# Kernel tuning notes

Hardware: AMD Instinct MI355X
Metric: run time of the kernel (lower is better)

The kernel has to match this reference:

```python
import jax, jax.numpy as jnp
import numpy as np

B, D_IN, D_OUT, DICT = 2048, 768, 768, 24576
TOP_K, TOP_K_AUX = 32, 512
L1_COEFF, AUX_PENALTY, N_DEAD = 0.001, 0.03125, 100.0


def setup_inputs() -> dict:
    key = jax.random.key(0)
    k1, k2, k3, k4, k5, k6 = jax.random.split(key, 6)
    x_in = jax.random.normal(k1, (B, D_IN), dtype=jnp.float32)
    y_target = jax.random.normal(k2, (B, D_OUT), dtype=jnp.float32)
    nb = jax.random.randint(k3, (DICT,), 0, 200).astype(jnp.float32)
    # kaiming-uniform-ish init
    bound_e = float(np.sqrt(6.0 / D_IN))
    W_enc = jax.random.uniform(k4, (D_IN, DICT), minval=-bound_e, maxval=bound_e, dtype=jnp.float32)
    bound_d = float(np.sqrt(6.0 / DICT))
    W_dec = jax.random.uniform(k5, (DICT, D_OUT), minval=-bound_d, maxval=bound_d, dtype=jnp.float32)
    W_dec = W_dec / jnp.linalg.norm(W_dec, axis=-1, keepdims=True)  # unit-norm rows
    b_dec = jnp.zeros((D_OUT,), dtype=jnp.float32)
    return {"x_in": x_in, "y_target": y_target, "num_batches_not_active": nb,
            "W_enc": W_enc, "W_dec": W_dec, "b_dec": b_dec}


def _unit_norm(x):
    m = x.mean(axis=-1, keepdims=True)
    x = x - m
    s = jnp.std(x, axis=-1, keepdims=True, ddof=1)  # torch .std is unbiased
    return x / (s + 1e-5), m, s


def reference(x_in, y_target, num_batches_not_active, W_enc, W_dec, b_dec):
    xn, _, _ = _unit_norm(x_in)
    yn, y_mean, y_std = _unit_norm(y_target)
    x_enc = xn - b_dec  # pre_enc_bias (input_size == output_size)
    acts = jax.nn.relu(x_enc @ W_enc)                      # [B, DICT]
    vals, idx = jax.lax.top_k(acts, TOP_K)                 # [B, TOP_K]
    rows = jnp.arange(B)[:, None]
    acts_sparse = jnp.zeros_like(acts).at[rows, idx].set(vals)
    y_pred = acts_sparse @ W_dec + b_dec                   # [B, D_OUT]
    y_pred_out = y_pred * y_std + y_mean

    # stateful dead-feature bookkeeping (update_inactive_features)
    col_active = acts_sparse.sum(axis=0) > 0
    nb = jnp.where(col_active, 0.0, num_batches_not_active + 1.0)

    l2_loss = jnp.mean((y_pred - yn) ** 2)
    l1_norm = jnp.mean(jnp.abs(acts_sparse).sum(axis=-1))
    l1_loss = L1_COEFF * l1_norm
    l0_norm = jnp.mean((acts_sparse > 0).astype(jnp.float32).sum(axis=-1))

    # auxiliary loss on dead features (static-shape masked top-k; masked cols
    # get -1 < relu acts so extras relu-clip to 0 -> same math as torch gather)
    dead = nb >= N_DEAD
    masked = jnp.where(dead[None, :], acts, -1.0)
    av, ai = jax.lax.top_k(masked, TOP_K_AUX)
    av = jax.nn.relu(av)
    acts_aux = jnp.zeros_like(acts).at[rows, ai].set(av)
    y_pred_aux = acts_aux @ W_dec
    residual = yn - y_pred
    l2_aux = AUX_PENALTY * jnp.mean((y_pred_aux - residual) ** 2)
    aux_loss = jnp.where(dead.any(), l2_aux, 0.0)

    loss = l2_loss + l1_loss + aux_loss
    num_dead_features = (nb > N_DEAD).sum()
    return (y_pred_out, acts_sparse, loss, l2_loss, l1_loss, l0_norm, l1_norm,
            aux_loss, num_dead_features)
```

## Files before the change

### kernel.cpp

```cpp
#include <hip/hip_runtime.h>
#include <math.h>

#define BATCH 2048
#define DIN 768
#define DICT 24576
#define KM 32
#define KA 512
#define NPT 48
#define L1_COEFF 0.001f
#define AUX_PENALTY 0.03125f
#define CAND_MAX 768
#define CAND_DELTA 0.08f
#define AUX_SPLIT 8
#define SAUX 18432
#define AGB ((DIN/128)*(BATCH/128)*AUX_SPLIT)

typedef __attribute__((ext_vector_type(8))) short bf16x8;
typedef __attribute__((ext_vector_type(8))) unsigned short u16x8;
typedef __attribute__((ext_vector_type(4))) float f32x4;

constexpr size_t WS_XENC   = 0;
constexpr size_t WS_YN     = WS_XENC + (size_t)BATCH*DIN;
constexpr size_t WS_YMEAN  = WS_YN + (size_t)BATCH*DIN;
constexpr size_t WS_YSTD   = WS_YMEAN + BATCH;
constexpr size_t WS_RES    = WS_YSTD + BATCH;
constexpr size_t WS_NSEL   = WS_RES + (size_t)BATCH*DIN;
constexpr size_t WS_SEL    = WS_NSEL + BATCH;
constexpr size_t WS_SELV   = WS_SEL + (size_t)BATCH*KM;
constexpr size_t WS_COLACT = WS_SELV + (size_t)BATCH*KM;
constexpr size_t WS_ACC    = WS_COLACT + DICT;
constexpr size_t WS_DB     = WS_ACC + 8;
constexpr size_t WS_XEB    = WS_DB + DICT/32;
constexpr size_t WS_WETF   = WS_XEB + (size_t)BATCH*DIN/2;
constexpr size_t WS_WETB   = WS_WETF + (size_t)DICT*DIN;
constexpr size_t WS_WDB    = WS_WETB + (size_t)DICT*DIN/2;
constexpr size_t WS_DPREF  = WS_XEB + DICT/32;
constexpr size_t WS_META   = WS_XEB + 2*(DICT/32);

__device__ __forceinline__ unsigned short f2b(float f){
    unsigned u = __float_as_uint(f);
    return (unsigned short)((u + 0x7fffu + ((u >> 16) & 1u)) >> 16);
}
__device__ __forceinline__ float b2f(unsigned short h){ return __uint_as_float(((unsigned)h) << 16); }

__device__ __forceinline__ void gld_lds16(const void* g, void* l){
    __builtin_amdgcn_global_load_lds(
        (const __attribute__((address_space(1))) unsigned int*)g,
        (__attribute__((address_space(3))) unsigned int*)l, 16, 0, 0);
}

__device__ __forceinline__ int blk_count512_w(int cw, int* s16, int par){
    if ((threadIdx.x & 63) == 0) s16[par*8 + (threadIdx.x >> 6)] = cw;
    __syncthreads();
    int tot = 0;
    #pragma unroll
    for (int w=0; w<8; w++) tot += s16[par*8+w];
    return tot;
}
__device__ __forceinline__ float blk_sum512(float v, float* s16, int par){
    #pragma unroll
    for (int off=32; off; off>>=1) v += __shfl_down(v, off);
    if ((threadIdx.x & 63) == 0) s16[par*8 + (threadIdx.x >> 6)] = v;
    __syncthreads();
    float t = 0.f;
    #pragma unroll
    for (int w=0; w<8; w++) t += s16[par*8+w];
    return t;
}
__device__ __forceinline__ float blk_sum256(float v, float* s8, int par){
    #pragma unroll
    for (int off=32; off; off>>=1) v += __shfl_down(v, off);
    if ((threadIdx.x & 63) == 0) s8[par*4 + (threadIdx.x >> 6)] = v;
    __syncthreads();
    float t = 0.f;
    #pragma unroll
    for (int w=0; w<4; w++) t += s8[par*4+w];
    return t;
}

__global__ __launch_bounds__(256) void prep_k(const float* __restrict__ x,
        const float* __restrict__ y, const float* __restrict__ bdec,
        const float* __restrict__ We, const float* __restrict__ Wd,
        float* __restrict__ Tf, unsigned short* __restrict__ Tb,
        unsigned short* __restrict__ Td, float* __restrict__ ws){
    __shared__ float s8[8];
    __shared__ float t1[32][33];
    __shared__ float t2[32][33];
    const int tid = threadIdx.x;
    if (blockIdx.x < 2*BATCH){
        int b = blockIdx.x; bool isy = b >= BATCH; int row = isy ? b - BATCH : b;
        if (b < 8){
            float* dst = ws + WS_COLACT;
            for (int i = b*256 + tid; i < DICT + 8; i += 2048) dst[i] = 0.f;
        }
        const float* src = (isy ? y : x) + (size_t)row*DIN;
        float v0 = src[tid], v1 = src[tid+256], v2 = src[tid+512];
        float s = blk_sum256(v0+v1+v2, s8, 0);
        float mean = s * (1.f/(float)DIN);
        float d0 = v0-mean, d1 = v1-mean, d2 = v2-mean;
        float vs = blk_sum256(d0*d0+d1*d1+d2*d2, s8, 1);
        float sd = sqrtf(vs / (float)(DIN-1));
        float inv = 1.f / (sd + 1e-5f);
        if (isy){
            float* yn = ws + WS_YN + (size_t)row*DIN;
            yn[tid] = d0*inv; yn[tid+256] = d1*inv; yn[tid+512] = d2*inv;
            if (tid==0){ ws[WS_YMEAN+row] = mean; ws[WS_YSTD+row] = sd; }
        } else {
            float* xe = ws + WS_XENC + (size_t)row*DIN;
            unsigned short* xeb = (unsigned short*)(ws + WS_XEB) + (size_t)row*DIN;
            float e0 = d0*inv - bdec[tid];
            float e1 = d1*inv - bdec[tid+256];
            float e2 = d2*inv - bdec[tid+512];
            xe[tid] = e0; xe[tid+256] = e1; xe[tid+512] = e2;
            xeb[tid] = f2b(e0); xeb[tid+256] = f2b(e1); xeb[tid+512] = f2b(e2);
        }
    } else {
        int t = blockIdx.x - 2*BATCH;
        int bx = t % (DICT/32), by = t / (DICT/32);
        int a0 = bx*32, k0 = by*32;
        int r = tid >> 5, c = tid & 31;
        #pragma unroll
        for (int rr=r; rr<32; rr+=8){
            t1[rr][c] = We[(size_t)(k0+rr)*DICT + a0 + c];
            t2[rr][c] = Wd[(size_t)(a0+rr)*DIN + k0 + c];
        }
        __syncthreads();
        #pragma unroll
        for (int rr=r; rr<32; rr+=8){
            float v = t1[c][rr];
            Tf[(size_t)(a0+rr)*DIN + k0 + c] = v;
            Tb[(size_t)(a0+rr)*DIN + k0 + c] = f2b(v);
            Td[(size_t)(k0+rr)*DICT + a0 + c] = f2b(t2[c][rr]);
        }
    }
}

__global__ __launch_bounds__(256) void gemm_mfma(const unsigned short* __restrict__ Abf,
        const unsigned short* __restrict__ Bbf, unsigned short* __restrict__ C){
    __shared__ __align__(16) unsigned short As[128*64];
    __shared__ __align__(16) unsigned short Bs[128*64];
    const int tid = threadIdx.x;
    const int w = tid >> 6, lane = tid & 63;
    const int g = blockIdx.x;
    const int xcd = g & 7;
    const int s_ = g >> 3;
    const int m_t = s_ & 15;
    const int n_t = xcd + 8*(s_ >> 4);
    const int m0 = m_t*128, n0 = n_t*128;
    const int srow = lane >> 3;
    const int schunk = (lane & 7) ^ srow;
    const int wm = (w >> 1)*64, wn = (w & 1)*64;
    f32x4 acc[16];
    #pragma unroll
    for (int i=0;i<16;i++) acc[i] = (f32x4){0.f,0.f,0.f,0.f};
    for (int kt = 0; kt < DIN; kt += 64){
        #pragma unroll
        for (int q=0;q<4;q++){
            int s = w*4 + q;
            int row = 8*s + srow;
            gld_lds16(Abf + (size_t)(m0+row)*DIN + kt + schunk*8, &As[8*s*64]);
            gld_lds16(Bbf + (size_t)(n0+row)*DIN + kt + schunk*8, &Bs[8*s*64]);
        }
        __syncthreads();
        #pragma unroll
        for (int kk=0; kk<64; kk+=32){
            bf16x8 af[4], bfr[4];
            int ch = (kk>>3) + (lane>>4);
            #pragma unroll
            for (int i=0;i<4;i++){
                int row = wm + i*16 + (lane&15);
                af[i] = *(const bf16x8*)&As[row*64 + ((ch ^ (row&7))<<3)];
            }
            #pragma unroll
            for (int j=0;j<4;j++){
                int row = wn + j*16 + (lane&15);
                bfr[j] = *(const bf16x8*)&Bs[row*64 + ((ch ^ (row&7))<<3)];
            }
            #pragma unroll
            for (int i=0;i<4;i++)
                #pragma unroll
                for (int j=0;j<4;j++)
                    acc[i*4+j] = __builtin_amdgcn_mfma_f32_16x16x32_bf16(af[i], bfr[j], acc[i*4+j], 0,0,0);
        }
        __syncthreads();
    }
    #pragma unroll
    for (int i=0;i<4;i++){
        #pragma unroll
        for (int r=0;r<4;r++){
            int m = m0 + wm + i*16 + (lane>>4)*4 + r;
            unsigned short* crow = C + (size_t)m*DICT + n0 + wn + (lane&15);
            #pragma unroll
            for (int j=0;j<4;j++)
                crow[j*16] = f2b(fmaxf(acc[i*4+j][r], 0.f) + 0.0f);
        }
    }
}

__global__ __launch_bounds__(512) void topk_main(const unsigned short* __restrict__ actsb,
        const float* __restrict__ WeTf, const float* __restrict__ Wdec,
        const float* __restrict__ bdec, float* __restrict__ ws,
        float* __restrict__ ypred_out){
    const int row = blockIdx.x, tid = threadIdx.x;
    const int lane = tid & 63, wid = tid >> 6;
    __shared__ float s_f16[16];
    __shared__ float s_x[DIN];
    __shared__ int   s_ci[CAND_MAX];
    __shared__ float s_cv[CAND_MAX];
    __shared__ int   s_li[KM];
    __shared__ float s_lv[KM];
    __shared__ int   s_n, s_m;
    const unsigned short* arow = actsb + (size_t)row * DICT;
    const float* xrow = ws + WS_XENC + (size_t)row * DIN;
    unsigned short h[NPT];
    #pragma unroll
    for (int i=0;i<6;i++){
        u16x8 v = *(const u16x8*)&arow[i*4096 + tid*8];
        #pragma unroll
        for (int e=0;e<8;e++) h[i*8+e] = v[e];
    }
    s_x[tid] = xrow[tid];
    if (tid < DIN-512) s_x[tid+512] = xrow[tid+512];
    if (tid == 0){ s_n = 0; s_m = 0; }

    unsigned prefix = 0;
    for (int bit=14; bit>=0; bit--){
        unsigned cand = prefix | (1u<<bit);
        int c = 0;
        #pragma unroll
        for (int q=0;q<NPT;q++) c += (int)__popcll(__ballot((unsigned)h[q] >= cand));
        if (c >= KM) prefix = cand;
    }
    float tc = b2f((unsigned short)prefix) - CAND_DELTA;
    __syncthreads();
    #pragma unroll
    for (int q=0;q<NPT;q++){
        if (b2f(h[q]) > tc){
            int p = atomicAdd(&s_n, 1);
            if (p < CAND_MAX) s_ci[p] = (q>>3)*4096 + tid*8 + (q&7);
        }
    }
    __syncthreads();
    int nc = s_n; if (nc > CAND_MAX) nc = CAND_MAX;
    for (int c = wid; c < nc; c += 8){
        const float* wr = WeTf + (size_t)s_ci[c]*DIN;
        float p = 0.f;
        #pragma unroll
        for (int t=0; t<12; t++) p = fmaf(s_x[lane + 64*t], wr[lane + 64*t], p);
        #pragma unroll
        for (int off=32; off; off>>=1) p += __shfl_down(p, off);
        if (lane == 0) s_cv[c] = fmaxf(p, 0.f);
    }
    __syncthreads();
    if (tid < nc){
        float vi = s_cv[tid]; int ii = s_ci[tid];
        int rank = 0;
        for (int j=0; j<nc; j++){
            float vj = s_cv[j];
            rank += (vj > vi) || (vj == vi && s_ci[j] < ii);
        }
        if (rank < KM){
            int p = atomicAdd(&s_m, 1);
            s_li[p] = ii; s_lv[p] = vi;
        }
    }
    __syncthreads();
    if (tid < KM){
        ((int*)ws)[WS_COLACT + s_li[tid]] = 1;
        ((int*)ws)[WS_SEL  + (size_t)row*KM + tid] = s_li[tid];
        ws[WS_SELV + (size_t)row*KM + tid] = s_lv[tid];
    }
    if (tid == 0){
        float l1 = 0.f; int l0 = 0;
        for (int l=0;l<KM;l++){ l1 += s_lv[l]; l0 += (s_lv[l] > 0.f); }
        atomicAdd(&ws[WS_ACC+1], l1);
        atomicAdd(&ws[WS_ACC+2], (float)l0);
    }
    __syncthreads();
    float ym = ws[WS_YMEAN+row], ys = ws[WS_YSTD+row];
    float l2loc = 0.f;
    for (int c = tid; c < DIN; c += 512){
        float acc = bdec[c];
        #pragma unroll 4
        for (int l=0;l<KM;l++) acc = fmaf(s_lv[l], Wdec[(size_t)s_li[l]*DIN + c], acc);
        float ynv = ws[WS_YN + (size_t)row*DIN + c];
        float d = acc - ynv;
        l2loc += d*d;
        ws[WS_RES + (size_t)row*DIN + c] = ynv - acc;
        ypred_out[(size_t)row*DIN + c] = fmaf(acc, ys, ym);
    }
    float l2t = blk_sum512(l2loc, s_f16, 0);
    if (tid==0) atomicAdd(&ws[WS_ACC+0], l2t);
}

__global__ __launch_bounds__(768) void deadscan_k(const float* __restrict__ nb,
        float* __restrict__ ws){
    __shared__ int s[DICT/32];
    __shared__ int c12[12];
    const int t = threadIdx.x;
    const int* colact = (const int*)ws + WS_COLACT;
    unsigned bits = 0; int cgt = 0;
    const int base = t*32;
    #pragma unroll 8
    for (int b=0;b<32;b++){
        int j = base + b;
        float nbn = colact[j] ? 0.f : nb[j] + 1.f;
        bits |= (nbn >= 100.f ? 1u : 0u) << b;
        cgt  += (nbn > 100.f) ? 1 : 0;
    }
    ((unsigned*)(ws + WS_DB))[t] = bits;
    int pc = __popc(bits);
    s[t] = pc;
    #pragma unroll
    for (int off=32; off; off>>=1) cgt += __shfl_down(cgt, off);
    if ((t & 63) == 0) c12[t >> 6] = cgt;
    __syncthreads();
    for (int off=1; off<DICT/32; off<<=1){
        int v = (t >= off) ? s[t-off] : 0;
        __syncthreads();
        s[t] += v;
        __syncthreads();
    }
    ((int*)(ws + WS_DPREF))[t] = s[t] - pc;
    if (t == DICT/32 - 1){
        int nd = s[t];
        int ndpad = (nd + 63) & ~63;
        if (ndpad > SAUX) ndpad = SAUX;
        int* meta = (int*)(ws + WS_META);
        meta[0] = nd; meta[1] = ndpad; meta[2] = ndpad >> 6;
        meta[3] = ((ndpad >> 6) + AUX_SPLIT - 1) / AUX_SPLIT;
        int tot = 0;
        #pragma unroll
        for (int wv=0; wv<12; wv++) tot += c12[wv];
        ws[WS_ACC+4] = (float)tot;
        ((int*)ws)[WS_ACC+5] = (nd > 0) ? 1 : 0;
    }
}

__global__ __launch_bounds__(512) void auxprep_k(const unsigned short* __restrict__ actsb,
        unsigned short* __restrict__ wdt, unsigned short* __restrict__ auxc,
        float* __restrict__ ws){
    __shared__ unsigned s_db[DICT/32];
    __shared__ int      s_dp[DICT/32];
    __shared__ int      s_i16[16];
    __shared__ unsigned short s_out[SAUX];
    const int tid = threadIdx.x;
    for (int i=tid; i<DICT/32; i+=512){
        s_db[i] = ((const unsigned*)(ws + WS_DB))[i];
        s_dp[i] = ((const int*)(ws + WS_DPREF))[i];
    }
    const int nd    = ((const int*)(ws + WS_META))[0];
    const int ndpad = ((const int*)(ws + WS_META))[1];
    __syncthreads();
    if (blockIdx.x < DIN){
        const int n = blockIdx.x;
        unsigned short* row = wdt + (size_t)n*DICT;
        #pragma unroll
        for (int i=0;i<6;i++){
            u16x8 a = *(const u16x8*)&row[i*4096 + tid*8];
            int w = i*128 + (tid>>2);
            unsigned dbw = s_db[w]; int dpw = s_dp[w];
            #pragma unroll
            for (int e=0;e<8;e++){
                int bit = (tid&3)*8 + e;
                if ((dbw >> bit) & 1u){
                    int p = dpw + __popc(dbw & ((1u<<bit)-1u));
                    if (p < SAUX) s_out[p] = a[e];
                }
            }
        }
        for (int t2 = nd + tid; t2 < ndpad; t2 += 512) s_out[t2] = 0;
        __syncthreads();
        for (int i = tid*8; i < ndpad; i += 4096)
            *(u16x8*)&row[i] = *(const u16x8*)&s_out[i];
    } else {
        const int row = blockIdx.x - DIN;
        const unsigned short* arow = actsb + (size_t)row * DICT;
        unsigned short key[NPT];
        #pragma unroll
        for (int i=0;i<6;i++){
            u16x8 v = *(const u16x8*)&arow[i*4096 + tid*8];
            unsigned dbw = s_db[i*128 + (tid>>2)];
            #pragma unroll
            for (int e=0;e<8;e++){
                unsigned short hv = v[e];
                key[i*8+e] = (((dbw >> ((tid&3)*8 + e)) & 1u) && hv) ? hv : 0;
            }
        }
        int par = 0;
        unsigned prefix = 0;
        for (int bit=14; bit>=0; bit--){
            unsigned cand = prefix | (1u<<bit);
            int c = 0;
            #pragma unroll
            for (int q=0;q<NPT;q++) c += (int)__popcll(__ballot((unsigned)key[q] >= cand));
            int tot = blk_count512_w(c, s_i16, par); par ^= 1;
            if (tot >= KA) prefix = cand;
        }
        unsigned thr = prefix ? prefix : 1u;
        #pragma unroll
        for (int i=0;i<6;i++){
            int w = i*128 + (tid>>2);
            unsigned dbw = s_db[w];
            int dpw = s_dp[w];
            #pragma unroll
            for (int e=0;e<8;e++){
                int bit = (tid&3)*8 + e;
                if ((dbw >> bit) & 1u){
                    int p = dpw + __popc(dbw & ((1u<<bit)-1u));
                    unsigned short kv = key[i*8+e];
                    if (p < SAUX) s_out[p] = ((unsigned)kv >= thr) ? kv : (unsigned short)0;
                }
            }
        }
        for (int t2 = nd + tid; t2 < ndpad; t2 += 512) s_out[t2] = 0;
        __syncthreads();
        unsigned short* crow = auxc + (size_t)row * SAUX;
        for (int i = tid*8; i < ndpad; i += 4096)
            *(u16x8*)&crow[i] = *(const u16x8*)&s_out[i];
    }
}

__global__ __launch_bounds__(256) void auxgz_k(const unsigned short* __restrict__ Abf,
        const unsigned short* __restrict__ Bbf, float* __restrict__ ws,
        float* __restrict__ acts){
    __shared__ __align__(16) unsigned short As[128*64];
    __shared__ __align__(16) unsigned short Bs[128*64];
    const int tid = threadIdx.x;
    if (blockIdx.x >= AGB){
        const int row = blockIdx.x - AGB;
        float4 z = make_float4(0.f,0.f,0.f,0.f);
        float4* arow4 = (float4*)(acts + (size_t)row*DICT);
        #pragma unroll
        for (int i=0;i<24;i++) arow4[tid + 256*i] = z;
        __syncthreads();
        if (tid < KM){
            int j   = ((const int*)ws)[WS_SEL + (size_t)row*KM + tid];
            float v = ws[WS_SELV + (size_t)row*KM + tid];
            (acts + (size_t)row*DICT)[j] = v;
        }
        return;
    }
    const int nkt   = ((const int*)(ws + WS_META))[2];
    const int chunk = ((const int*)(ws + WS_META))[3];
    const int g = blockIdx.x;
    const int z = g & 7;
    const int s_ = g >> 3;
    const int m_t = s_ & 15;
    const int n_t = s_ >> 4;
    int t0 = z * chunk;
    int t1 = t0 + chunk; if (t1 > nkt) t1 = nkt;
    const int w = tid >> 6, lane = tid & 63;
    const int m0 = m_t*128, n0 = n_t*128;
    const int srow = lane >> 3;
    const int schunk = (lane & 7) ^ srow;
    const int wm = (w >> 1)*64, wn = (w & 1)*64;
    f32x4 acc[16];
    #pragma unroll
    for (int i=0;i<16;i++) acc[i] = (f32x4){0.f,0.f,0.f,0.f};
    for (int t = t0; t < t1; ++t){
        int kt = t*64;
        #pragma unroll
        for (int q=0;q<4;q++){
            int s = w*4 + q;
            int row = 8*s + srow;
            gld_lds16(Abf + (size_t)(m0+row)*SAUX + kt + schunk*8, &As[8*s*64]);
            gld_lds16(Bbf + (size_t)(n0+row)*DICT + kt + schunk*8, &Bs[8*s*64]);
        }
        __syncthreads();
        #pragma unroll
        for (int kk=0; kk<64; kk+=32){
            bf16x8 af[4], bfr[4];
            int ch = (kk>>3) + (lane>>4);
            #pragma unroll
            for (int i=0;i<4;i++){
                int row = wm + i*16 + (lane&15);
                af[i] = *(const bf16x8*)&As[row*64 + ((ch ^ (row&7))<<3)];
            }
            #pragma unroll
            for (int j=0;j<4;j++){
                int row = wn + j*16 + (lane&15);
                bfr[j] = *(const bf16x8*)&Bs[row*64 + ((ch ^ (row&7))<<3)];
            }
            #pragma unroll
            for (int i=0;i<4;i++)
                #pragma unroll
                for (int j=0;j<4;j++)
                    acc[i*4+j] = __builtin_amdgcn_mfma_f32_16x16x32_bf16(af[i], bfr[j], acc[i*4+j], 0,0,0);
        }
        __syncthreads();
    }
    float* buf = ws + ((z < 6) ? (WS_WETB + (size_t)z*BATCH*DIN)
                               : (z == 6 ? WS_YN : WS_XENC));
    #pragma unroll
    for (int i=0;i<4;i++){
        #pragma unroll
        for (int r=0;r<4;r++){
            int m = m0 + wm + i*16 + (lane>>4)*4 + r;
            float* crow = buf + (size_t)m*DIN + n0 + wn + (lane&15);
            #pragma unroll
            for (int j=0;j<4;j++) crow[j*16] = acc[i*4+j][r];
        }
    }
}

__global__ __launch_bounds__(256) void auxloss_k(float* __restrict__ ws){
    __shared__ float s8[8];
    const float4* b0 = (const float4*)(ws + WS_WETB);
    const float4* b1 = (const float4*)(ws + WS_WETB + 1*(size_t)BATCH*DIN);
    const float4* b2 = (const float4*)(ws + WS_WETB + 2*(size_t)BATCH*DIN);
    const float4* b3 = (const float4*)(ws + WS_WETB + 3*(size_t)BATCH*DIN);
    const float4* b4 = (const float4*)(ws + WS_WETB + 4*(size_t)BATCH*DIN);
    const float4* b5 = (const float4*)(ws + WS_WETB + 5*(size_t)BATCH*DIN);
    const float4* b6 = (const float4*)(ws + WS_YN);
    const float4* b7 = (const float4*)(ws + WS_XENC);
    const float4* r4 = (const float4*)(ws + WS_RES);
    float s = 0.f;
    const size_t n4 = (size_t)BATCH*DIN/4;
    for (size_t i = (size_t)blockIdx.x*256 + threadIdx.x; i < n4; i += (size_t)gridDim.x*256){
        float4 a0 = b0[i], a1 = b1[i], a2 = b2[i], a3 = b3[i];
        float4 a4 = b4[i], a5 = b5[i], a6 = b6[i], a7 = b7[i];
        float4 rr = r4[i];
        float x0 = ((a0.x+a1.x)+(a2.x+a3.x))+((a4.x+a5.x)+(a6.x+a7.x)) - rr.x;
        float x1 = ((a0.y+a1.y)+(a2.y+a3.y))+((a4.y+a5.y)+(a6.y+a7.y)) - rr.y;
        float x2 = ((a0.z+a1.z)+(a2.z+a3.z))+((a4.z+a5.z)+(a6.z+a7.z)) - rr.z;
        float x3 = ((a0.w+a1.w)+(a2.w+a3.w))+((a4.w+a5.w)+(a6.w+a7.w)) - rr.w;
        s += x0*x0 + x1*x1 + x2*x2 + x3*x3;
    }
    float tot = blk_sum256(s, s8, 0);
    if (threadIdx.x == 0) atomicAdd(&ws[WS_ACC+3], tot);
}

__global__ void finalize_k(const float* __restrict__ ws, float* __restrict__ out){
    if (threadIdx.x == 0){
        float l2   = ws[WS_ACC+0] / (float)((size_t)BATCH*DIN);
        float l1n  = ws[WS_ACC+1] / (float)BATCH;
        float l1l  = L1_COEFF * l1n;
        float l0   = ws[WS_ACC+2] / (float)BATCH;
        float auxm = AUX_PENALTY * (ws[WS_ACC+3] / (float)((size_t)BATCH*DIN));
        int any    = ((const int*)ws)[WS_ACC+5];
        float auxl = any ? auxm : 0.f;
        out[0] = l2 + l1l + auxl;
        out[1] = l2;
        out[2] = l1l;
        out[3] = l0;
        out[4] = l1n;
        out[5] = auxl;
        out[6] = ws[WS_ACC+4];
    }
}

extern "C" void kernel_launch(void* const* d_in, const int* in_sizes, int n_in,
                              void* d_out, int out_size, void* d_ws, size_t ws_size,
                              hipStream_t stream){
    const float* x_in = (const float*)d_in[0];
    const float* y_t  = (const float*)d_in[1];
    const float* nb   = (const float*)d_in[2];
    const float* Wenc = (const float*)d_in[3];
    const float* Wdec = (const float*)d_in[4];
    const float* bdec = (const float*)d_in[5];
    float* out  = (float*)d_out;
    float* ws   = (float*)d_ws;
    float* acts = out + (size_t)BATCH*DIN;
    float* scal = out + (size_t)BATCH*DIN + (size_t)BATCH*DICT;
    unsigned short* actsb = (unsigned short*)acts;

    unsigned short* xeb  = (unsigned short*)(ws + WS_XEB);
    float*          wetf = ws + WS_WETF;
    unsigned short* wetb = (unsigned short*)(ws + WS_WETB);
    unsigned short* wdt  = (unsigned short*)(ws + WS_WDB);
    unsigned short* auxc = (unsigned short*)(ws + WS_WETF);

    prep_k<<<2*BATCH + (DICT/32)*(DIN/32), 256, 0, stream>>>(
        x_in, y_t, bdec, Wenc, Wdec, wetf, wetb, wdt, ws);
    gemm_mfma<<<(DICT/128)*(BATCH/128), 256, 0, stream>>>(xeb, wetb, actsb);
    topk_main<<<BATCH, 512, 0, stream>>>(actsb, wetf, Wdec, bdec, ws, out);
    deadscan_k<<<1, DICT/32, 0, stream>>>(nb, ws);
    auxprep_k<<<DIN + BATCH, 512, 0, stream>>>(actsb, wdt, auxc, ws);
    auxgz_k<<<AGB + BATCH, 256, 0, stream>>>(auxc, wdt, ws, acts);
    auxloss_k<<<256, 256, 0, stream>>>(ws);
    finalize_k<<<1, 64, 0, stream>>>(ws, scal);
}
```

Baseline: 1.041 ms.

## Use block-wide radix threshold for top-k candidates and fuse dead-feature scan

The radix search for the top-k threshold now counts across the whole 512-thread block instead of per wave. This gives a tighter candidate threshold, so the candidate buffer shrinks from 768 to 128 and far fewer fp32 dot-product recomputations are needed. The separate single-block dead-feature scan kernel is removed; its work now runs in whichever topk_main block finishes last, detected with an atomic counter and thread fences. The cost is a block reduction in each of the 15 bit iterations, and the fused scan depends on that counter being zeroed before every launch.

```diff
diff --git a/kernel.cpp b/kernel.cpp
--- a/kernel.cpp
+++ b/kernel.cpp
@@ -9,7 +9,7 @@
 #define NPT 48
 #define L1_COEFF 0.001f
 #define AUX_PENALTY 0.03125f
-#define CAND_MAX 768
+#define CAND_MAX 128
 #define CAND_DELTA 0.08f
 #define AUX_SPLIT 8
 #define SAUX 18432
@@ -199,17 +199,19 @@
 
 __global__ __launch_bounds__(512) void topk_main(const unsigned short* __restrict__ actsb,
         const float* __restrict__ WeTf, const float* __restrict__ Wdec,
-        const float* __restrict__ bdec, float* __restrict__ ws,
-        float* __restrict__ ypred_out){
+        const float* __restrict__ bdec, const float* __restrict__ nb,
+        float* __restrict__ ws, float* __restrict__ ypred_out){
     const int row = blockIdx.x, tid = threadIdx.x;
     const int lane = tid & 63, wid = tid >> 6;
+    __shared__ int   s_i16[16];
     __shared__ float s_f16[16];
     __shared__ float s_x[DIN];
     __shared__ int   s_ci[CAND_MAX];
     __shared__ float s_cv[CAND_MAX];
     __shared__ int   s_li[KM];
     __shared__ float s_lv[KM];
-    __shared__ int   s_n, s_m;
+    __shared__ int   s_scan[DICT/32];
+    __shared__ int   s_n, s_m, s_last;
     const unsigned short* arow = actsb + (size_t)row * DICT;
     const float* xrow = ws + WS_XENC + (size_t)row * DIN;
     unsigned short h[NPT];
@@ -223,16 +225,17 @@
     if (tid < DIN-512) s_x[tid+512] = xrow[tid+512];
     if (tid == 0){ s_n = 0; s_m = 0; }
 
+    int par = 0;
     unsigned prefix = 0;
     for (int bit=14; bit>=0; bit--){
         unsigned cand = prefix | (1u<<bit);
         int c = 0;
         #pragma unroll
         for (int q=0;q<NPT;q++) c += (int)__popcll(__ballot((unsigned)h[q] >= cand));
-        if (c >= KM) prefix = cand;
+        int tot = blk_count512_w(c, s_i16, par); par ^= 1;
+        if (tot >= KM) prefix = cand;
     }
     float tc = b2f((unsigned short)prefix) - CAND_DELTA;
-    __syncthreads();
     #pragma unroll
     for (int q=0;q<NPT;q++){
         if (b2f(h[q]) > tc){
@@ -291,39 +294,60 @@
     }
     float l2t = blk_sum512(l2loc, s_f16, 0);
     if (tid==0) atomicAdd(&ws[WS_ACC+0], l2t);
-}
-
-__global__ __launch_bounds__(768) void deadscan_k(const float* __restrict__ nb,
-        float* __restrict__ ws){
-    __shared__ int s[DICT/32];
-    __shared__ int c12[12];
-    const int t = threadIdx.x;
+
+    __threadfence();
+    if (tid == 0){
+        int prev = atomicAdd((int*)ws + WS_ACC + 6, 1);
+        s_last = (prev == BATCH-1) ? 1 : 0;
+    }
+    __syncthreads();
+    if (!s_last) return;
+    __threadfence();
     const int* colact = (const int*)ws + WS_COLACT;
-    unsigned bits = 0; int cgt = 0;
-    const int base = t*32;
-    #pragma unroll 8
-    for (int b=0;b<32;b++){
-        int j = base + b;
-        float nbn = colact[j] ? 0.f : nb[j] + 1.f;
-        bits |= (nbn >= 100.f ? 1u : 0u) << b;
-        cgt  += (nbn > 100.f) ? 1 : 0;
-    }
-    ((unsigned*)(ws + WS_DB))[t] = bits;
-    int pc = __popc(bits);
-    s[t] = pc;
+    const int i1 = tid, i2 = 512 + tid;
+    unsigned bits1 = 0, bits2 = 0; int cgt = 0, pc1 = 0, pc2 = 0;
+    {
+        int base = i1*32;
+        #pragma unroll 8
+        for (int b=0;b<32;b++){
+            int j = base + b;
+            float nbn = colact[j] ? 0.f : nb[j] + 1.f;
+            bits1 |= (nbn >= 100.f ? 1u : 0u) << b;
+            cgt  += (nbn > 100.f) ? 1 : 0;
+        }
+        pc1 = __popc(bits1);
+        ((unsigned*)(ws + WS_DB))[i1] = bits1;
+        s_scan[i1] = pc1;
+    }
+    if (tid < 256){
+        int base = i2*32;
+        #pragma unroll 8
+        for (int b=0;b<32;b++){
+            int j = base + b;
+            float nbn = colact[j] ? 0.f : nb[j] + 1.f;
+            bits2 |= (nbn >= 100.f ? 1u : 0u) << b;
+            cgt  += (nbn > 100.f) ? 1 : 0;
+        }
+        pc2 = __popc(bits2);
+        ((unsigned*)(ws + WS_DB))[i2] = bits2;
+        s_scan[i2] = pc2;
+    }
     #pragma unroll
     for (int off=32; off; off>>=1) cgt += __shfl_down(cgt, off);
-    if ((t & 63) == 0) c12[t >> 6] = cgt;
+    if (lane == 0) s_i16[wid] = cgt;
     __syncthreads();
     for (int off=1; off<DICT/32; off<<=1){
-        int v = (t >= off) ? s[t-off] : 0;
-        __syncthreads();
-        s[t] += v;
-        __syncthreads();
-    }
-    ((int*)(ws + WS_DPREF))[t] = s[t] - pc;
-    if (t == DICT/32 - 1){
-        int nd = s[t];
+        int v1 = (i1 >= off) ? s_scan[i1-off] : 0;
+        int v2 = (tid < 256 && i2 >= off) ? s_scan[i2-off] : 0;
+        __syncthreads();
+        s_scan[i1] += v1;
+        if (tid < 256) s_scan[i2] += v2;
+        __syncthreads();
+    }
+    ((int*)(ws + WS_DPREF))[i1] = s_scan[i1] - pc1;
+    if (tid < 256) ((int*)(ws + WS_DPREF))[i2] = s_scan[i2] - pc2;
+    if (tid == 0){
+        int nd = s_scan[DICT/32 - 1];
         int ndpad = (nd + 63) & ~63;
         if (ndpad > SAUX) ndpad = SAUX;
         int* meta = (int*)(ws + WS_META);
@@ -331,7 +355,7 @@
         meta[3] = ((ndpad >> 6) + AUX_SPLIT - 1) / AUX_SPLIT;
         int tot = 0;
         #pragma unroll
-        for (int wv=0; wv<12; wv++) tot += c12[wv];
+        for (int wv=0; wv<8; wv++) tot += s_i16[wv];
         ws[WS_ACC+4] = (float)tot;
         ((int*)ws)[WS_ACC+5] = (nd > 0) ? 1 : 0;
     }
@@ -574,8 +598,7 @@
     prep_k<<<2*BATCH + (DICT/32)*(DIN/32), 256, 0, stream>>>(
         x_in, y_t, bdec, Wenc, Wdec, wetf, wetb, wdt, ws);
     gemm_mfma<<<(DICT/128)*(BATCH/128), 256, 0, stream>>>(xeb, wetb, actsb);
-    topk_main<<<BATCH, 512, 0, stream>>>(actsb, wetf, Wdec, bdec, ws, out);
-    deadscan_k<<<1, DICT/32, 0, stream>>>(nb, ws);
+    topk_main<<<BATCH, 512, 0, stream>>>(actsb, wetf, Wdec, bdec, nb, ws, out);
     auxprep_k<<<DIN + BATCH, 512, 0, stream>>>(actsb, wdt, auxc, ws);
     auxgz_k<<<AGB + BATCH, 256, 0, stream>>>(auxc, wdt, ws, acts);
     auxloss_k<<<256, 256, 0, stream>>>(ws);
```

Result: slower. 1.435 ms (+37.9%).
